# Optimization experiments

Hardware: AMD Instinct MI355X
Metric: run time of the kernel (lower is better)

The kernel has to match this reference:

```python
import jax, jax.numpy as jnp
import numpy as np

BN_EPS = 1e-5


def _gcn_norm(edge_index, n):
    # PyG gcn_norm with add_self_loops=True: deg counts in-degree incl. self loop
    loops = jnp.arange(n, dtype=edge_index.dtype)
    src = jnp.concatenate([edge_index[0], loops])
    dst = jnp.concatenate([edge_index[1], loops])
    deg = jax.ops.segment_sum(jnp.ones(src.shape[0], jnp.float32), dst, num_segments=n)
    dinv = jnp.where(deg > 0, jax.lax.rsqrt(jnp.maximum(deg, 1.0)), 0.0)
    norm = dinv[src] * dinv[dst]  # [E + N]
    return src, dst, norm


def _gcn_conv(x, src, dst, norm, W, b, n):
    h = x @ W                      # dense transform first (fewer FLOPs: d_out gather)
    msgs = h[src] * norm[:, None]  # [E+N, d_out] gathered, degree-normalized
    return jax.ops.segment_sum(msgs, dst, num_segments=n) + b


def _bn_relu(x, gamma, beta):
    # BatchNorm1d in training mode: biased batch stats over node dim
    mu = x.mean(axis=0)
    var = x.var(axis=0)
    return jax.nn.relu(gamma * (x - mu) * jax.lax.rsqrt(var + BN_EPS) + beta)


def setup_inputs() -> dict:
    key = jax.random.key(0)
    ks = jax.random.split(key, 8)
    N, E, D_IN, H1, H2, D_OUT = 50000, 500000, 128, 256, 512, 128
    x = jax.random.normal(ks[0], (N, D_IN), jnp.float32)
    edge_index = jax.random.randint(ks[1], (2, E), 0, N, jnp.int64)
    def lin(k, fan_in, fan_out):
        bound = 1.0 / np.sqrt(fan_in)
        kw, kb = jax.random.split(k)
        W = jax.random.uniform(kw, (fan_in, fan_out), jnp.float32, -bound, bound)
        b = jax.random.uniform(kb, (fan_out,), jnp.float32, -bound, bound)
        return W, b
    W1, b1 = lin(ks[2], D_IN, H1)
    W2, b2 = lin(ks[3], H1, H2)
    Wl, bl = lin(ks[4], H2, D_OUT)
    return {
        "x": x, "edge_index": edge_index,
        "W1": W1, "b1": b1, "gamma1": jnp.ones((H1,), jnp.float32), "beta1": jnp.zeros((H1,), jnp.float32),
        "W2": W2, "b2": b2, "gamma2": jnp.ones((H2,), jnp.float32), "beta2": jnp.zeros((H2,), jnp.float32),
        "Wl": Wl, "bl": bl,
    }


def reference(x, edge_index, W1, b1, gamma1, beta1, W2, b2, gamma2, beta2, Wl, bl):
    n = x.shape[0]
    src, dst, norm = _gcn_norm(edge_index, n)
    h = _bn_relu(_gcn_conv(x, src, dst, norm, W1, b1, n), gamma1, beta1)
    h = _bn_relu(_gcn_conv(h, src, dst, norm, W2, b2, n), gamma2, beta2)
    return h @ Wl + bl
```

## Files before the change

kernel.cpp:

```cpp
#include <hip/hip_runtime.h>
#include <cstdint>
#include <cstddef>

typedef __bf16 bf16;
typedef bf16 bf16x2 __attribute__((ext_vector_type(2)));
typedef bf16 bf16x4 __attribute__((ext_vector_type(4)));
typedef bf16 bf16x8 __attribute__((ext_vector_type(8)));
typedef float f32x4 __attribute__((ext_vector_type(4)));

__global__ void k_init(int* __restrict__ deg, int* __restrict__ cur,
                       float* __restrict__ sums1, float* __restrict__ sums2, int N) {
  int i = blockIdx.x * 256 + threadIdx.x;
  if (i < N) { deg[i] = 1; cur[i] = 0; }
  if (i < 512)  sums1[i] = 0.f;
  if (i < 1024) sums2[i] = 0.f;
}

__global__ void k_count(const int* __restrict__ ei, int* __restrict__ deg, int E) {
  int e = blockIdx.x * 256 + threadIdx.x;
  if (e < E) atomicAdd(&deg[ei[E + e]], 1);
}

__global__ __launch_bounds__(256) void k_scan1(const int* __restrict__ deg,
                                               int* __restrict__ bsum, int N) {
  int t = threadIdx.x;
  int i = blockIdx.x * 256 + t;
  int v = (i < N) ? deg[i] - 1 : 0;
#pragma unroll
  for (int off = 32; off > 0; off >>= 1) v += __shfl_down(v, off, 64);
  __shared__ int red[4];
  if ((t & 63) == 0) red[t >> 6] = v;
  __syncthreads();
  if (t == 0) bsum[blockIdx.x] = red[0] + red[1] + red[2] + red[3];
}

__global__ __launch_bounds__(256) void k_scan2(const int* __restrict__ bsum,
                                               int* __restrict__ bpre, int B) {
  __shared__ int s[256];
  int t = threadIdx.x;
  int v = (t < B) ? bsum[t] : 0;
  s[t] = v;
  __syncthreads();
  for (int off = 1; off < 256; off <<= 1) {
    int add = (t >= off) ? s[t - off] : 0;
    __syncthreads();
    s[t] += add;
    __syncthreads();
  }
  if (t < B) bpre[t] = s[t] - v;
}

__global__ __launch_bounds__(256) void k_scan3(const int* __restrict__ deg,
                                               const int* __restrict__ bpre,
                                               int* __restrict__ roff,
                                               float* __restrict__ dinv, int N) {
  __shared__ int s[256];
  int t = threadIdx.x;
  int i = blockIdx.x * 256 + t;
  int d = (i < N) ? deg[i] : 1;
  int v = d - 1;
  if (i >= N) v = 0;
  s[t] = v;
  __syncthreads();
  for (int off = 1; off < 256; off <<= 1) {
    int add = (t >= off) ? s[t - off] : 0;
    __syncthreads();
    s[t] += add;
    __syncthreads();
  }
  if (i < N) {
    int base = bpre[blockIdx.x];
    roff[i] = base + s[t] - v;
    dinv[i] = rsqrtf((float)d);
    if (i == N - 1) roff[N] = base + s[t];
  }
}

__global__ void k_scatter(const int* __restrict__ ei, const int* __restrict__ roff,
                          int* __restrict__ cur, int* __restrict__ csr, int E) {
  int e = blockIdx.x * 256 + threadIdx.x;
  if (e >= E) return;
  int d = ei[E + e];
  int p = atomicAdd(&cur[d], 1);
  csr[roff[d] + p] = ei[e];
}

__global__ void k_cvt_x(const float* __restrict__ x, bf16* __restrict__ xb, size_t total) {
  size_t base = ((size_t)blockIdx.x * 256 + threadIdx.x) * 4;
  if (base >= total) return;
  const float4 v = *(const float4*)(x + base);
  bf16x4 o;
  o[0] = (bf16)v.x; o[1] = (bf16)v.y; o[2] = (bf16)v.z; o[3] = (bf16)v.w;
  *(bf16x4*)(xb + base) = o;
}

__global__ void k_cvt_w(const float* __restrict__ W1, const float* __restrict__ W2,
                        const float* __restrict__ Wl, bf16* __restrict__ w1t,
                        bf16* __restrict__ w2t, bf16* __restrict__ wlt) {
  int i = blockIdx.x * 256 + threadIdx.x;
  if (i < 32768) {
    int n = i >> 7, k = i & 127;
    w1t[i] = (bf16)W1[(size_t)k * 256 + n];
  } else if (i < 163840) {
    int j = i - 32768;
    int n = j >> 8, k = j & 255;
    w2t[j] = (bf16)W2[(size_t)k * 512 + n];
  } else {
    int j = i - 163840;
    int n = j >> 9, k = j & 511;
    wlt[j] = (bf16)Wl[(size_t)k * 128 + n];
  }
}

template<int K, int NOUT, bool FINAL>
__global__ __launch_bounds__(256) void k_gemm(const bf16* __restrict__ A,
                                              const bf16* __restrict__ Bt,
                                              bf16* __restrict__ outB,
                                              float* __restrict__ outF,
                                              const float* __restrict__ bias,
                                              float* __restrict__ sums,
                                              int Mreal) {
  __shared__ uint4 lA[512];
  __shared__ uint4 lB[512];
  const int tid = threadIdx.x;
  const int wv = tid >> 6, lane = tid & 63;
  const int q = lane >> 4, mr = lane & 15;
  const int m0 = blockIdx.x * 128;
  const int n0 = blockIdx.y * 128;
  const int rw = (wv >> 1) * 64, cw = (wv & 1) * 64;

  const int r0 = tid >> 2, j0 = tid & 3;
  const bf16* gA0 = A + (size_t)(m0 + r0) * K + j0 * 8;
  const bf16* gA1 = A + (size_t)(m0 + 64 + r0) * K + j0 * 8;
  const bf16* gB0 = Bt + (size_t)(n0 + r0) * K + j0 * 8;
  const bf16* gB1 = Bt + (size_t)(n0 + 64 + r0) * K + j0 * 8;
  const int sl0 = j0 * 128 + r0;
  const int sl1 = j0 * 128 + 64 + r0;

  f32x4 acc[4][4];
#pragma unroll
  for (int r = 0; r < 4; ++r)
#pragma unroll
    for (int c = 0; c < 4; ++c) acc[r][c] = (f32x4){0.f, 0.f, 0.f, 0.f};

  uint4 pA0 = *(const uint4*)(gA0);
  uint4 pA1 = *(const uint4*)(gA1);
  uint4 pB0 = *(const uint4*)(gB0);
  uint4 pB1 = *(const uint4*)(gB1);

  for (int k0 = 0; k0 < K; k0 += 32) {
    uint4 nA0 = pA0, nA1 = pA1, nB0 = pB0, nB1 = pB1;
    if (k0 + 32 < K) {
      nA0 = *(const uint4*)(gA0 + k0 + 32);
      nA1 = *(const uint4*)(gA1 + k0 + 32);
      nB0 = *(const uint4*)(gB0 + k0 + 32);
      nB1 = *(const uint4*)(gB1 + k0 + 32);
    }
    __syncthreads();
    lA[sl0] = pA0; lA[sl1] = pA1;
    lB[sl0] = pB0; lB[sl1] = pB1;
    __syncthreads();
    bf16x8 af[4], bfr[4];
#pragma unroll
    for (int r = 0; r < 4; ++r)
      af[r] = ((const bf16x8*)lA)[q * 128 + rw + r * 16 + mr];
#pragma unroll
    for (int c = 0; c < 4; ++c)
      bfr[c] = ((const bf16x8*)lB)[q * 128 + cw + c * 16 + mr];
#pragma unroll
    for (int r = 0; r < 4; ++r)
#pragma unroll
      for (int c = 0; c < 4; ++c)
        acc[r][c] = __builtin_amdgcn_mfma_f32_16x16x32_bf16(af[r], bfr[c], acc[r][c], 0, 0, 0);
    pA0 = nA0; pA1 = nA1; pB0 = nB0; pB1 = nB1;
  }

#pragma unroll
  for (int c = 0; c < 4; ++c) {
    const int col = n0 + cw + c * 16 + mr;
    float s0 = 0.f, s1 = 0.f;
#pragma unroll
    for (int r = 0; r < 4; ++r) {
#pragma unroll
      for (int i = 0; i < 4; ++i) {
        int row = m0 + rw + r * 16 + q * 4 + i;
        float v = acc[r][c][i];
        if (FINAL) {
          if (row < Mreal) outF[(size_t)row * NOUT + col] = v + bias[col];
        } else {
          outB[(size_t)row * NOUT + col] = (bf16)v;
          if (row < Mreal) { s0 += v; s1 += v * v; }
        }
      }
    }
    if (!FINAL) {
      s0 += __shfl_xor(s0, 16, 64); s0 += __shfl_xor(s0, 32, 64);
      s1 += __shfl_xor(s1, 16, 64); s1 += __shfl_xor(s1, 32, 64);
      if (q == 0) { atomicAdd(&sums[col], s0); atomicAdd(&sums[NOUT + col], s1); }
    }
  }
}

template<int C, bool BN>
__global__ __launch_bounds__(256) void k_agg(const bf16* __restrict__ h,
                                             bf16* __restrict__ g,
                                             const int* __restrict__ csr,
                                             const int* __restrict__ roff,
                                             const float* __restrict__ dinv,
                                             const float* __restrict__ scale,
                                             const float* __restrict__ shift,
                                             int N) {
  constexpr int VPL = C / 64;
  const int lane = threadIdx.x & 63;
  const int v = (int)(((unsigned)blockIdx.x * 256 + threadIdx.x) >> 6);
  if (v >= N) return;
  float sc[VPL], sh[VPL];
  if constexpr (BN) {
#pragma unroll
    for (int u = 0; u < VPL; ++u) { sc[u] = scale[lane * VPL + u]; sh[u] = shift[lane * VPL + u]; }
  }
  const float dv = dinv[v];
  float acc[VPL];
#pragma unroll
  for (int u = 0; u < VPL; ++u) acc[u] = 0.f;

  auto accum = [&](int src, float w) {
    const bf16* hr = h + (size_t)src * C + lane * VPL;
    float vals[VPL];
    if constexpr (VPL == 2) {
      bf16x2 t = *(const bf16x2*)hr;
      vals[0] = (float)t[0]; vals[1] = (float)t[1];
    } else {
      bf16x4 t = *(const bf16x4*)hr;
#pragma unroll
      for (int u = 0; u < 4; ++u) vals[u] = (float)t[u];
    }
#pragma unroll
    for (int u = 0; u < VPL; ++u) {
      float xx = vals[u];
      if constexpr (BN) xx = fmaxf(0.f, xx * sc[u] + sh[u]);
      acc[u] += w * xx;
    }
  };

  accum(v, dv);
  const int beg = roff[v], end = roff[v + 1];
  for (int base = beg; base < end; base += 64) {
    int cnt = min(64, end - base);
    int s = 0; float w = 0.f;
    if (lane < cnt) { s = csr[base + lane]; w = dinv[s]; }
    for (int j = 0; j < cnt; ++j) {
      int sj = __shfl(s, j, 64);
      float wj = __shfl(w, j, 64);
      accum(sj, wj);
    }
  }

  bf16* gv = g + (size_t)v * C + lane * VPL;
  if constexpr (VPL == 2) {
    bf16x2 o;
    o[0] = (bf16)(acc[0] * dv); o[1] = (bf16)(acc[1] * dv);
    *(bf16x2*)gv = o;
  } else {
    bf16x4 o;
#pragma unroll
    for (int u = 0; u < 4; ++u) o[u] = (bf16)(acc[u] * dv);
    *(bf16x4*)gv = o;
  }
}

__global__ void k_bnfinal(const float* __restrict__ sums, const float* __restrict__ gamma,
                          const float* __restrict__ beta, float* __restrict__ scale,
                          float* __restrict__ shift, int C, float invN) {
  int c = blockIdx.x * 256 + threadIdx.x;
  if (c >= C) return;
  float mu = sums[c] * invN;
  float var = sums[C + c] * invN - mu * mu;
  float is = rsqrtf(var + 1e-5f);
  float sc = gamma[c] * is;
  scale[c] = sc;
  shift[c] = beta[c] - mu * sc;
}

template<int C>
__global__ void k_bnapply(bf16* __restrict__ g, const float* __restrict__ scale,
                          const float* __restrict__ shift, size_t total) {
  size_t base = ((size_t)blockIdx.x * 256 + threadIdx.x) * 8;
  if (base >= total) return;
  int col = (int)(base & (size_t)(C - 1));
  bf16x8 t = *(const bf16x8*)(g + base);
  bf16x8 o;
#pragma unroll
  for (int j = 0; j < 8; ++j)
    o[j] = (bf16)fmaxf(0.f, (float)t[j] * scale[col + j] + shift[col + j]);
  *(bf16x8*)(g + base) = o;
}

extern "C" void kernel_launch(void* const* d_in, const int* in_sizes, int n_in,
                              void* d_out, int out_size, void* d_ws, size_t ws_size,
                              hipStream_t stream) {
  const float* x   = (const float*)d_in[0];
  const int*   ei  = (const int*)d_in[1];
  const float* W1  = (const float*)d_in[2];
  const float* g1  = (const float*)d_in[4];
  const float* be1 = (const float*)d_in[5];
  const float* W2  = (const float*)d_in[6];
  const float* g2  = (const float*)d_in[8];
  const float* be2 = (const float*)d_in[9];
  const float* Wl  = (const float*)d_in[10];
  const float* bl  = (const float*)d_in[11];
  float* out = (float*)d_out;

  const int N  = in_sizes[0] / 128;
  const int E  = in_sizes[1] / 2;
  const int Mp = ((N + 127) / 128) * 128;
  const int NB = (N + 255) / 256;

  char* p = (char*)d_ws;
  auto carve = [&](size_t bytes) { void* r = (void*)p; p += (bytes + 255) & ~(size_t)255; return r; };
  int*   deg   = (int*)carve(sizeof(int) * N);
  int*   cur   = (int*)carve(sizeof(int) * N);
  int*   roff  = (int*)carve(sizeof(int) * (N + 1));
  int*   csr   = (int*)carve(sizeof(int) * E);
  int*   bsum  = (int*)carve(sizeof(int) * 256);
  int*   bpre  = (int*)carve(sizeof(int) * 256);
  float* dinv  = (float*)carve(sizeof(float) * N);
  float* sums1 = (float*)carve(sizeof(float) * 512);
  float* sums2 = (float*)carve(sizeof(float) * 1024);
  float* sc1   = (float*)carve(sizeof(float) * 256);
  float* sh1   = (float*)carve(sizeof(float) * 256);
  float* sc2   = (float*)carve(sizeof(float) * 512);
  float* sh2   = (float*)carve(sizeof(float) * 512);
  bf16*  w1t   = (bf16*)carve(sizeof(bf16) * 256 * 128);
  bf16*  w2t   = (bf16*)carve(sizeof(bf16) * 512 * 256);
  bf16*  wlt   = (bf16*)carve(sizeof(bf16) * 128 * 512);
  bf16*  xb    = (bf16*)carve(sizeof(bf16) * (size_t)Mp * 128);
  bf16*  ax1   = (bf16*)carve(sizeof(bf16) * (size_t)Mp * 128);
  bf16*  t1    = (bf16*)carve(sizeof(bf16) * (size_t)Mp * 256);
  bf16*  ax2   = (bf16*)carve(sizeof(bf16) * (size_t)Mp * 256);
  bf16*  t2    = (bf16*)carve(sizeof(bf16) * (size_t)Mp * 512);
  (void)n_in; (void)out_size; (void)ws_size;

  const int gE = (E + 255) / 256;
  k_init<<<NB, 256, 0, stream>>>(deg, cur, sums1, sums2, N);
  k_count<<<gE, 256, 0, stream>>>(ei, deg, E);
  k_scan1<<<NB, 256, 0, stream>>>(deg, bsum, N);
  k_scan2<<<1, 256, 0, stream>>>(bsum, bpre, NB);
  k_scan3<<<NB, 256, 0, stream>>>(deg, bpre, roff, dinv, N);
  k_scatter<<<gE, 256, 0, stream>>>(ei, roff, cur, csr, E);

  k_cvt_x<<<(int)(((size_t)N * 128 / 4 + 255) / 256), 256, 0, stream>>>(x, xb, (size_t)N * 128);
  k_cvt_w<<<896, 256, 0, stream>>>(W1, W2, Wl, w1t, w2t, wlt);

  const int gAgg = (N + 3) / 4;
  k_agg<128, false><<<gAgg, 256, 0, stream>>>(xb, ax1, csr, roff, dinv, nullptr, nullptr, N);
  k_gemm<128, 256, false><<<dim3(Mp / 128, 2), 256, 0, stream>>>(ax1, w1t, t1, nullptr, nullptr, sums1, N);
  k_bnfinal<<<1, 256, 0, stream>>>(sums1, g1, be1, sc1, sh1, 256, 1.f / (float)N);

  k_agg<256, true><<<gAgg, 256, 0, stream>>>(t1, ax2, csr, roff, dinv, sc1, sh1, N);
  k_gemm<256, 512, false><<<dim3(Mp / 128, 4), 256, 0, stream>>>(ax2, w2t, t2, nullptr, nullptr, sums2, N);
  k_bnfinal<<<2, 256, 0, stream>>>(sums2, g2, be2, sc2, sh2, 512, 1.f / (float)N);
  k_bnapply<512><<<(int)(((size_t)Mp * 512 / 8 + 255) / 256), 256, 0, stream>>>(t2, sc2, sh2, (size_t)Mp * 512);

  k_gemm<512, 128, true><<<dim3(Mp / 128, 1), 256, 0, stream>>>(t2, wlt, nullptr, out, bl, nullptr, N);
}
```

Measured before the change: 390.7 us.

## Double-buffer and XOR-swizzle GEMM LDS tiles, use 64-row tiles for final GEMM

The GEMM kernel now keeps two LDS buffers per operand, so each k-step needs one barrier instead of two. LDS rows are XOR-swizzled by k-chunk to cut bank conflicts on the MFMA fragment loads. The final output GEMM uses 64-row M tiles, which doubles its block count to raise occupancy on the narrow 128-column output. The risks are extra LDS footprint and per-wave work too small to amortize loads in the final GEMM.

```diff
diff --git a/kernel.cpp b/kernel.cpp
--- a/kernel.cpp
+++ b/kernel.cpp
@@ -120,55 +120,64 @@
                                               const float* __restrict__ bias,
                                               float* __restrict__ sums,
                                               int Mreal) {
-  __shared__ uint4 lA[512];
-  __shared__ uint4 lB[512];
+  constexpr int MT  = FINAL ? 64 : 128;
+  constexpr int RPW = MT / 32;
+  __shared__ uint4 lA[2][MT * 4];
+  __shared__ uint4 lB[2][512];
   const int tid = threadIdx.x;
   const int wv = tid >> 6, lane = tid & 63;
   const int q = lane >> 4, mr = lane & 15;
-  const int m0 = blockIdx.x * 128;
+  const int m0 = blockIdx.x * MT;
   const int n0 = blockIdx.y * 128;
-  const int rw = (wv >> 1) * 64, cw = (wv & 1) * 64;
+  const int rw = (wv >> 1) * (MT / 2), cw = (wv & 1) * 64;
 
   const int r0 = tid >> 2, j0 = tid & 3;
-  const bf16* gA0 = A + (size_t)(m0 + r0) * K + j0 * 8;
+  const bf16* gA0 = A + (size_t)(m0 + (MT == 64 ? r0 : r0)) * K + j0 * 8;
   const bf16* gA1 = A + (size_t)(m0 + 64 + r0) * K + j0 * 8;
   const bf16* gB0 = Bt + (size_t)(n0 + r0) * K + j0 * 8;
   const bf16* gB1 = Bt + (size_t)(n0 + 64 + r0) * K + j0 * 8;
-  const int sl0 = j0 * 128 + r0;
-  const int sl1 = j0 * 128 + 64 + r0;
-
-  f32x4 acc[4][4];
-#pragma unroll
-  for (int r = 0; r < 4; ++r)
+  const int swz = j0 << 1;
+  const int slA0 = j0 * MT + (r0 ^ swz);
+  const int slA1 = j0 * MT + ((r0 + 64) ^ swz);
+  const int slB0 = j0 * 128 + (r0 ^ swz);
+  const int slB1 = j0 * 128 + ((r0 + 64) ^ swz);
+
+  f32x4 acc[RPW][4];
+#pragma unroll
+  for (int r = 0; r < RPW; ++r)
 #pragma unroll
     for (int c = 0; c < 4; ++c) acc[r][c] = (f32x4){0.f, 0.f, 0.f, 0.f};
 
   uint4 pA0 = *(const uint4*)(gA0);
-  uint4 pA1 = *(const uint4*)(gA1);
+  uint4 pA1, pB1;
+  if constexpr (MT == 128) pA1 = *(const uint4*)(gA1);
   uint4 pB0 = *(const uint4*)(gB0);
-  uint4 pB1 = *(const uint4*)(gB1);
-
-  for (int k0 = 0; k0 < K; k0 += 32) {
+  pB1 = *(const uint4*)(gB1);
+
+  const int qs = q << 1;
+  int buf = 0;
+  for (int k0 = 0; k0 < K; k0 += 32, buf ^= 1) {
     uint4 nA0 = pA0, nA1 = pA1, nB0 = pB0, nB1 = pB1;
     if (k0 + 32 < K) {
       nA0 = *(const uint4*)(gA0 + k0 + 32);
-      nA1 = *(const uint4*)(gA1 + k0 + 32);
+      if constexpr (MT == 128) nA1 = *(const uint4*)(gA1 + k0 + 32);
       nB0 = *(const uint4*)(gB0 + k0 + 32);
       nB1 = *(const uint4*)(gB1 + k0 + 32);
     }
-    __syncthreads();
-    lA[sl0] = pA0; lA[sl1] = pA1;
-    lB[sl0] = pB0; lB[sl1] = pB1;
-    __syncthreads();
-    bf16x8 af[4], bfr[4];
-#pragma unroll
-    for (int r = 0; r < 4; ++r)
-      af[r] = ((const bf16x8*)lA)[q * 128 + rw + r * 16 + mr];
+    lA[buf][slA0] = pA0;
+    if constexpr (MT == 128) lA[buf][slA1] = pA1;
+    lB[buf][slB0] = pB0;
+    lB[buf][slB1] = pB1;
+    __syncthreads();
+    bf16x8 af[RPW], bfr[4];
+#pragma unroll
+    for (int r = 0; r < RPW; ++r)
+      af[r] = ((const bf16x8*)lA[buf])[q * MT + ((rw + r * 16 + mr) ^ qs)];
 #pragma unroll
     for (int c = 0; c < 4; ++c)
-      bfr[c] = ((const bf16x8*)lB)[q * 128 + cw + c * 16 + mr];
-#pragma unroll
-    for (int r = 0; r < 4; ++r)
+      bfr[c] = ((const bf16x8*)lB[buf])[q * 128 + ((cw + c * 16 + mr) ^ qs)];
+#pragma unroll
+    for (int r = 0; r < RPW; ++r)
 #pragma unroll
       for (int c = 0; c < 4; ++c)
         acc[r][c] = __builtin_amdgcn_mfma_f32_16x16x32_bf16(af[r], bfr[c], acc[r][c], 0, 0, 0);
@@ -180,7 +189,7 @@
     const int col = n0 + cw + c * 16 + mr;
     float s0 = 0.f, s1 = 0.f;
 #pragma unroll
-    for (int r = 0; r < 4; ++r) {
+    for (int r = 0; r < RPW; ++r) {
 #pragma unroll
       for (int i = 0; i < 4; ++i) {
         int row = m0 + rw + r * 16 + q * 4 + i;
@@ -362,5 +371,5 @@
   k_bnfinal<<<2, 256, 0, stream>>>(sums2, g2, be2, sc2, sh2, 512, 1.f / (float)N);
   k_bnapply<512><<<(int)(((size_t)Mp * 512 / 8 + 255) / 256), 256, 0, stream>>>(t2, sc2, sh2, (size_t)Mp * 512);
 
-  k_gemm<512, 128, true><<<dim3(Mp / 128, 1), 256, 0, stream>>>(t2, wlt, nullptr, out, bl, nullptr, N);
-}
+  k_gemm<512, 128, true><<<dim3(Mp / 64, 1), 256, 0, stream>>>(t2, wlt, nullptr, out, bl, nullptr, N);
+}
```

Result: faster. 382.9 us (-2.0%).
